# Kernel optimization log

Hardware: AMD Instinct MI355X
Metric: run time of the kernel (lower is better)

## Reference

```python
import jax, jax.numpy as jnp
import numpy as np

FFT_LENGTH = 2048
HOP_LENGTH = 512  # window_length // 4, window_length == fft_length


def _hann_periodic(n):
    # tf.signal.hann_window(n, periodic=True)
    return (0.5 - 0.5 * jnp.cos(2.0 * jnp.pi * jnp.arange(n) / n)).astype(jnp.float32)


def setup_inputs() -> dict:
    key = jax.random.key(0)
    k1, k2 = jax.random.split(key)
    B, F, NB = 4, 4000, FFT_LENGTH // 2 + 1
    spec_real = jax.random.normal(k1, (B, F, NB), dtype=jnp.float32)
    spec_imag = jax.random.normal(k2, (B, F, NB), dtype=jnp.float32)
    return {"spec_real": spec_real, "spec_imag": spec_imag}


def reference(spec_real, spec_imag) -> jnp.ndarray:
    fft_length, hop = FFT_LENGTH, HOP_LENGTH
    B, F, _ = spec_real.shape
    window = _hann_periodic(fft_length)  # [N], window_length == fft_length so no padding

    # irfft of the complex spectrogram -> time-domain frames [B, F, N]
    frames = jnp.fft.irfft(spec_real + 1j * spec_imag, n=fft_length).astype(jnp.float32)
    windowed = window * frames  # [B, F, N]

    # overlap-and-add: output length L = (F-1)*hop + N
    L = (F - 1) * hop + fft_length
    idx = (jnp.arange(F) * hop)[:, None] + jnp.arange(fft_length)[None, :]  # [F, N]
    out = jnp.zeros((B, L), jnp.float32).at[:, idx].add(windowed)

    # librosa window_sumsquare: overlap-add of squared window, guard tiny values
    wsq = jnp.zeros((L,), jnp.float32).at[idx].add(window * window)
    tiny = jnp.float32(np.finfo(np.float32).tiny)
    window_sum = jnp.where(wsq > tiny, wsq, jnp.float32(1.0))

    y = out / window_sum
    # center=True: trim fft_length//2 on each side
    half = fft_length // 2
    return y[:, half:L - half]
```

## Files before the change

kernel.cpp:

```cpp
#include <hip/hip_runtime.h>
#include <math.h>

#define NB       1025
#define M        1024
#define FFTN     2048
#define HOP      512
#define NFRAMES  4000
#define BATCH    4
#define OUT_T    2047488
#define R_HOPS   8
#define REG_PB   501
#define PI_F     3.14159265358979323846f

__device__ __forceinline__ float2 cmul(float2 a, float2 b) {
    return make_float2(a.x*b.x - a.y*b.y, a.x*b.y + a.y*b.x);
}
__device__ __forceinline__ float4 cmul4(float4 v, float2 w) {
    return make_float4(v.x*w.x - v.y*w.y, v.x*w.y + v.y*w.x,
                       v.z*w.x - v.w*w.y, v.z*w.y + v.w*w.x);
}
__device__ __forceinline__ float4 f4add(float4 a, float4 b){ return make_float4(a.x+b.x, a.y+b.y, a.z+b.z, a.w+b.w); }
__device__ __forceinline__ float4 f4sub(float4 a, float4 b){ return make_float4(a.x-b.x, a.y-b.y, a.z-b.z, a.w-b.w); }
__device__ __forceinline__ float4 f4addi(float4 a, float4 b){ return make_float4(a.x-b.y, a.y+b.x, a.z-b.w, a.w+b.z); }
__device__ __forceinline__ float4 f4subi(float4 a, float4 b){ return make_float4(a.x+b.y, a.y-b.x, a.z+b.w, a.w-b.z); }

__device__ __forceinline__ int SW4(int i) { return i ^ ((i >> 3) & 7); }

__device__ __forceinline__ float wsq_at(int p) {
    int u  = p + FFTN / 2;
    int fm = u >> 9;
    int n0 = u & 511;
    float wsq = 0.f;
    #pragma unroll
    for (int jj = 0; jj < 4; ++jj) {
        int fr = fm - jj;
        if (fr >= 0 && fr < NFRAMES) {
            int n = n0 + (jj << 9);
            float sw = __sinf((PI_F / (float)FFTN) * (float)n);
            float w  = sw * sw;
            wsq += w * w;
        }
    }
    const float tiny = 1.17549435e-38f;
    return (wsq > tiny) ? wsq : 1.0f;
}
__device__ __forceinline__ float invw_at(int p, bool edge) {
    if (edge && (p < 512 || p >= OUT_T - 512)) return 1.0f / wsq_at(p);
    return (2.0f / 3.0f);
}

template<int ST>
__device__ __forceinline__ void stage4x(const float4* __restrict__ src,
                                        float4* __restrict__ dst, int j, float2 w1) {
    const int Ns = 1 << (2 * ST);
    float4 v0 = src[SW4(j)];
    float4 v1 = src[SW4(j + 256)];
    float4 v2 = src[SW4(j + 512)];
    float4 v3 = src[SW4(j + 768)];
    float2 w2 = cmul(w1, w1);
    float2 w3 = cmul(w2, w1);
    v1 = cmul4(v1, w1); v2 = cmul4(v2, w2); v3 = cmul4(v3, w3);
    float4 t0 = f4add(v0, v2), t1 = f4sub(v0, v2);
    float4 t2 = f4add(v1, v3), t3 = f4sub(v1, v3);
    int jm = j & (Ns - 1);
    int idxD = ((j >> (2 * ST)) << (2 * ST + 2)) + jm;
    dst[SW4(idxD         )] = f4add(t0, t2);
    dst[SW4(idxD +     Ns)] = f4addi(t1, t3);
    dst[SW4(idxD + 2 * Ns)] = f4sub(t0, t2);
    dst[SW4(idxD + 3 * Ns)] = f4subi(t1, t3);
}

__device__ __forceinline__ void load_spec(const float* __restrict__ sr,
                                          const float* __restrict__ si,
                                          int b, int f, int j,
                                          float* car, float* cai,
                                          float* cbr, float* cbi) {
    const size_t fb = ((size_t)b * NFRAMES + f) * NB;
    const float* __restrict__ xr = sr + fb;
    const float* __restrict__ xi = si + fb;
    #pragma unroll
    for (int kk = 0; kk < 4; ++kk) {
        int k  = j + kk * 256;
        int mk = M - k;
        car[kk] = xr[k];  cai[kk] = xi[k];
        cbr[kk] = xr[mk]; cbi[kk] = xi[mk];
    }
}

__device__ __forceinline__ void pack2_st0(float4* __restrict__ dst, int j,
                                          const float2* twp,
                                          const float* a1r, const float* a1i,
                                          const float* b1r, const float* b1i,
                                          const float* a2r, const float* a2i,
                                          const float* b2r, const float* b2i) {
    float4 z[4];
    #pragma unroll
    for (int kk = 0; kk < 4; ++kk) {
        float ar = a1r[kk], ai = a1i[kk], br = b1r[kk], bi = b1i[kk];
        float cr = a2r[kk], ci = a2i[kk], dr = b2r[kk], di = b2i[kk];
        if (kk == 0 && j == 0) { ai = 0.f; bi = 0.f; ci = 0.f; di = 0.f; }
        float2 t = twp[kk];
        float Er = 0.5f*(ar+br), Ei = 0.5f*(ai-bi), Dr = 0.5f*(ar-br), Di = 0.5f*(ai+bi);
        float Or = Dr*t.x - Di*t.y, Oi = Dr*t.y + Di*t.x;
        float Fr = 0.5f*(cr+dr), Fi = 0.5f*(ci-di), Gr = 0.5f*(cr-dr), Gi = 0.5f*(ci+di);
        float Pr = Gr*t.x - Gi*t.y, Pi = Gr*t.y + Gi*t.x;
        z[kk] = make_float4(Er - Oi, Ei + Or, Fr - Pi, Fi + Pr);
    }
    float4 t0 = f4add(z[0], z[2]), t1 = f4sub(z[0], z[2]);
    float4 t2 = f4add(z[1], z[3]), t3 = f4sub(z[1], z[3]);
    dst[SW4(4*j    )] = f4add(t0, t2);
    dst[SW4(4*j + 1)] = f4addi(t1, t3);
    dst[SW4(4*j + 2)] = f4sub(t0, t2);
    dst[SW4(4*j + 3)] = f4subi(t1, t3);
}

__global__ __launch_bounds__(256) void istft_rpair_kernel(
    const float* __restrict__ sr, const float* __restrict__ si,
    float* __restrict__ out)
{
    __shared__ float4 buf0[M];
    __shared__ float4 buf1[M];

    const int blk = blockIdx.x;
    const int b   = blk / REG_PB;
    const int reg = blk - b * REG_PB;
    const int s0h = reg * R_HOPS;
    const int j   = threadIdx.x;
    const bool edge = (reg == 0) || (reg == REG_PB - 1);

    float2 tw_pack[4];
    #pragma unroll
    for (int kk = 0; kk < 4; ++kk) {
        int k = j + kk * 256;
        float s, c;
        __sincosf(PI_F * (float)k * (1.0f / (float)M), &s, &c);
        tw_pack[kk] = make_float2(c, s);
    }
    float2 w1s[4];
    #pragma unroll
    for (int st = 1; st <= 4; ++st) {
        int Ns = 1 << (2 * st);
        int jm = j & (Ns - 1);
        float ang = (0.5f * PI_F / (float)Ns) * (float)jm;
        float s1, c1;
        __sincosf(ang, &s1, &c1);
        w1s[st-1] = make_float2(c1, s1);
    }
    float wreg[4][2];
    #pragma unroll
    for (int q = 0; q < 4; ++q) {
        int n = j + q * 256;
        #pragma unroll
        for (int h = 0; h < 2; ++h) {
            int t = 2 * n + h;
            float swv = __sinf((PI_F / (float)FFTN) * (float)t);
            wreg[q][h] = swv * swv * (1.0f / 1024.0f);
        }
    }

    float2 Acc[R_HOPS];
    #pragma unroll
    for (int s = 0; s < R_HOPS; ++s) Acc[s] = make_float2(0.f, 0.f);

    const int fbase = s0h - 3;

    #pragma unroll
    for (int t = 0; t < 6; ++t) {
        const int fA = fbase + 2 * t;
        const int fB = fA + 1;
        const bool vA = (fA >= 0) && (fA < NFRAMES);
        const bool vB = (t < 5) && (fB >= 0) && (fB < NFRAMES);
        if (!vA && !vB) continue;

        int fAc = fA < 0 ? 0 : (fA > NFRAMES-1 ? NFRAMES-1 : fA);
        int fBc = fB < 0 ? 0 : (fB > NFRAMES-1 ? NFRAMES-1 : fB);

        float a1r[4], a1i[4], b1r[4], b1i[4];
        float a2r[4], a2i[4], b2r[4], b2i[4];
        load_spec(sr, si, b, fAc, j, a1r, a1i, b1r, b1i);
        load_spec(sr, si, b, fBc, j, a2r, a2i, b2r, b2i);

        pack2_st0(buf0, j, tw_pack, a1r, a1i, b1r, b1i, a2r, a2i, b2r, b2i);
        __syncthreads();
        stage4x<1>(buf0, buf1, j, w1s[0]);
        __syncthreads();
        stage4x<2>(buf1, buf0, j, w1s[1]);
        __syncthreads();
        stage4x<3>(buf0, buf1, j, w1s[2]);
        __syncthreads();

        {
            float4 v0 = buf1[SW4(j)];
            float4 v1 = buf1[SW4(j + 256)];
            float4 v2 = buf1[SW4(j + 512)];
            float4 v3 = buf1[SW4(j + 768)];
            float2 w1 = w1s[3];
            float2 w2 = cmul(w1, w1);
            float2 w3 = cmul(w2, w1);
            v1 = cmul4(v1, w1); v2 = cmul4(v2, w2); v3 = cmul4(v3, w3);
            float4 t0 = f4add(v0, v2), t1 = f4sub(v0, v2);
            float4 t2 = f4add(v1, v3), t3 = f4sub(v1, v3);
            float4 g[4];
            g[0] = f4add(t0, t2);
            g[1] = f4addi(t1, t3);
            g[2] = f4sub(t0, t2);
            g[3] = f4subi(t1, t3);
            if (vA) {
                #pragma unroll
                for (int q = 0; q < 4; ++q) {
                    const int s = 2 * t - 3 + q;
                    if (s >= 0 && s < R_HOPS) {
                        Acc[s].x += g[q].x * wreg[q][0];
                        Acc[s].y += g[q].y * wreg[q][1];
                    }
                }
            }
            if (vB) {
                #pragma unroll
                for (int q = 0; q < 4; ++q) {
                    const int s = 2 * t - 2 + q;
                    if (s >= 0 && s < R_HOPS) {
                        Acc[s].x += g[q].z * wreg[q][0];
                        Acc[s].y += g[q].w * wreg[q][1];
                    }
                }
            }
        }
    }

    float* outb = out + (size_t)b * OUT_T;
    const int base_u = s0h * HOP;
    #pragma unroll
    for (int s = 0; s < R_HOPS; ++s) {
        int i2 = j + 256 * s;
        int p0 = base_u + 2 * i2 - FFTN / 2;
        int p1 = p0 + 1;
        if ((unsigned)p0 < (unsigned)OUT_T) outb[p0] = Acc[s].x * invw_at(p0, edge);
        if ((unsigned)p1 < (unsigned)OUT_T) outb[p1] = Acc[s].y * invw_at(p1, edge);
    }
}

extern "C" void kernel_launch(void* const* d_in, const int* in_sizes, int n_in,
                              void* d_out, int out_size, void* d_ws, size_t ws_size,
                              hipStream_t stream) {
    const float* sr = (const float*)d_in[0];
    const float* si = (const float*)d_in[1];
    float* out = (float*)d_out;
    istft_rpair_kernel<<<BATCH * REG_PB, 256, 0, stream>>>(sr, si, out);
}
```

Before: 57.40 us.

## Double hops per workgroup to cut halo FFT recomputation and remap blocks per XCD

Each workgroup now produces 16 output hops (two adjacent regions) instead of 8. It runs 10 frame-pair iterations instead of 6, so the overlapping halo frames are inverse-FFT'd fewer times in total. Block IDs are also remapped so consecutive logical blocks land on the same XCD, which may improve L2 locality of the shared frames. The cost is twice the accumulator registers, half as many workgroups, and a longer serial loop per block.

```diff
diff --git a/kernel.cpp b/kernel.cpp
--- a/kernel.cpp
+++ b/kernel.cpp
@@ -9,7 +9,9 @@
 #define BATCH    4
 #define OUT_T    2047488
 #define R_HOPS   8
-#define REG_PB   501
+#define NPAIR    251
+#define NWG      (BATCH * NPAIR)
+#define CHOPS    16
 #define PI_F     3.14159265358979323846f
 
 __device__ __forceinline__ float2 cmul(float2 a, float2 b) {
@@ -114,19 +116,27 @@
     dst[SW4(4*j + 3)] = f4subi(t1, t3);
 }
 
-__global__ __launch_bounds__(256) void istft_rpair_kernel(
+__global__ __launch_bounds__(256) void istft_pair_kernel(
     const float* __restrict__ sr, const float* __restrict__ si,
     float* __restrict__ out)
 {
     __shared__ float4 buf0[M];
     __shared__ float4 buf1[M];
 
-    const int blk = blockIdx.x;
-    const int b   = blk / REG_PB;
-    const int reg = blk - b * REG_PB;
-    const int s0h = reg * R_HOPS;
-    const int j   = threadIdx.x;
-    const bool edge = (reg == 0) || (reg == REG_PB - 1);
+    int blk;
+    {
+        const int o   = blockIdx.x;
+        const int xcd = o & 7, k = o >> 3;
+        const int q = NWG / 8, r = NWG % 8;
+        blk = (xcd < r ? xcd * (q + 1) : r * (q + 1) + (xcd - r) * q) + k;
+    }
+
+    const int b    = blk / NPAIR;
+    const int pr   = blk - b * NPAIR;
+    const int regA = 2 * pr;
+    const int s0hA = regA * R_HOPS;
+    const int j    = threadIdx.x;
+    const bool edge = (regA == 0) || (regA == 500);
 
     float2 tw_pack[4];
     #pragma unroll
@@ -158,18 +168,18 @@
         }
     }
 
-    float2 Acc[R_HOPS];
-    #pragma unroll
-    for (int s = 0; s < R_HOPS; ++s) Acc[s] = make_float2(0.f, 0.f);
-
-    const int fbase = s0h - 3;
-
-    #pragma unroll
-    for (int t = 0; t < 6; ++t) {
+    float2 Acc[CHOPS];
+    #pragma unroll
+    for (int s = 0; s < CHOPS; ++s) Acc[s] = make_float2(0.f, 0.f);
+
+    const int fbase = s0hA - 3;
+
+    #pragma unroll
+    for (int t = 0; t < 10; ++t) {
         const int fA = fbase + 2 * t;
         const int fB = fA + 1;
         const bool vA = (fA >= 0) && (fA < NFRAMES);
-        const bool vB = (t < 5) && (fB >= 0) && (fB < NFRAMES);
+        const bool vB = (t < 9) && (fB >= 0) && (fB < NFRAMES);
         if (!vA && !vB) continue;
 
         int fAc = fA < 0 ? 0 : (fA > NFRAMES-1 ? NFRAMES-1 : fA);
@@ -209,7 +219,7 @@
                 #pragma unroll
                 for (int q = 0; q < 4; ++q) {
                     const int s = 2 * t - 3 + q;
-                    if (s >= 0 && s < R_HOPS) {
+                    if (s >= 0 && s < CHOPS) {
                         Acc[s].x += g[q].x * wreg[q][0];
                         Acc[s].y += g[q].y * wreg[q][1];
                     }
@@ -219,7 +229,7 @@
                 #pragma unroll
                 for (int q = 0; q < 4; ++q) {
                     const int s = 2 * t - 2 + q;
-                    if (s >= 0 && s < R_HOPS) {
+                    if (s >= 0 && s < CHOPS) {
                         Acc[s].x += g[q].z * wreg[q][0];
                         Acc[s].y += g[q].w * wreg[q][1];
                     }
@@ -229,9 +239,9 @@
     }
 
     float* outb = out + (size_t)b * OUT_T;
-    const int base_u = s0h * HOP;
-    #pragma unroll
-    for (int s = 0; s < R_HOPS; ++s) {
+    const int base_u = s0hA * HOP;
+    #pragma unroll
+    for (int s = 0; s < CHOPS; ++s) {
         int i2 = j + 256 * s;
         int p0 = base_u + 2 * i2 - FFTN / 2;
         int p1 = p0 + 1;
@@ -246,5 +256,5 @@
     const float* sr = (const float*)d_in[0];
     const float* si = (const float*)d_in[1];
     float* out = (float*)d_out;
-    istft_rpair_kernel<<<BATCH * REG_PB, 256, 0, stream>>>(sr, si, out);
-}
+    istft_pair_kernel<<<NWG, 256, 0, stream>>>(sr, si, out);
+}
```

Result: faster. 49.91 us, median of 2 (-13.0%).
